# Optimization experiments

Measured on AMD Instinct MI355X. Metric: run time of the kernel, lower is better.

The kernel has to match this reference:

```python
import jax, jax.numpy as jnp
import numpy as np

B, S, D, H, L, I, V, T = 8, 512, 768, 12, 6, 3072, 30522, 2
DH = D // H  # 64


def ln2d(x, g, b, eps=1e-5):
    # LayerNorm over the last two dims ([S, D]), affine params shaped [S, D]
    mu = jnp.mean(x, axis=(-2, -1), keepdims=True)
    var = jnp.var(x, axis=(-2, -1), keepdims=True)
    return (x - mu) * jax.lax.rsqrt(var + eps) * g + b


def setup_inputs() -> dict:
    key = jax.random.key(0)
    ks = jax.random.split(key, 16)
    s = 0.02
    inp = {
        "input_ids": jax.random.randint(ks[0], (B, S), 0, V, dtype=jnp.int32),
        "segment_ids": jax.random.randint(ks[1], (B, S), 0, T, dtype=jnp.int32),
        "input_mask": jnp.ones((B, S), dtype=jnp.float32),
        "word_emb": jax.random.normal(ks[2], (V, D), jnp.float32) * s,
        "seg_emb": jax.random.normal(ks[3], (T, D), jnp.float32) * s,
        "pos_emb": jax.random.normal(ks[4], (S, D), jnp.float32) * s,
        "ln0_g": jnp.ones((S, D), jnp.float32),
        "ln0_b": jnp.zeros((S, D), jnp.float32),
        "Wq": jax.random.normal(ks[5], (L, D, D), jnp.float32) * s,
        "Wk": jax.random.normal(ks[6], (L, D, D), jnp.float32) * s,
        "Wv": jax.random.normal(ks[7], (L, D, D), jnp.float32) * s,
        "W1": jax.random.normal(ks[8], (L, D, D), jnp.float32) * s,
        "b1": jnp.zeros((L, D), jnp.float32),
        "Wi": jax.random.normal(ks[9], (L, D, I), jnp.float32) * s,
        "bi": jnp.zeros((L, I), jnp.float32),
        "W2": jax.random.normal(ks[10], (L, I, D), jnp.float32) * s,
        "b2": jnp.zeros((L, D), jnp.float32),
        "lng": jnp.ones((L, S, D), jnp.float32),
        "lnb": jnp.zeros((L, S, D), jnp.float32),
        "Wp": jax.random.normal(ks[11], (D, 2), jnp.float32) * s,
        "bp": jnp.zeros((2,), jnp.float32),
    }
    return inp


def _forward(input_ids, segment_ids, input_mask, word_emb, seg_emb, pos_emb,
             ln0_g, ln0_b, Wq, Wk, Wv, W1, b1, Wi, bi, W2, b2, lng, lnb, Wp, bp):
    # embedding (word + segment + position), then 2-D LayerNorm
    x = word_emb[input_ids] + seg_emb[segment_ids] + pos_emb  # [B,S,D]
    x = ln2d(x, ln0_g, ln0_b)
    # multiplicative attention mask, broadcast over heads and KEY axis
    qmask = input_mask[:, None, :, None]  # [B,1,S,1]
    scale = 1.0 / jnp.sqrt(jnp.asarray(DH, x.dtype))
    for l in range(L):
        prev = x
        q = (x @ Wq[l]).reshape(B, S, H, DH).transpose(0, 2, 1, 3)
        k = (x @ Wk[l]).reshape(B, S, H, DH).transpose(0, 2, 1, 3)
        v = (x @ Wv[l]).reshape(B, S, H, DH).transpose(0, 2, 1, 3)
        scores = jnp.einsum('bhqd,bhkd->bhqk', q, k) * scale
        scores = scores * qmask  # multiplicative mask (as in source)
        probs = jax.nn.softmax(scores, axis=-1)
        attn = jnp.einsum('bhqk,bhkd->bhqd', probs, v)
        attn = attn.transpose(0, 2, 1, 3).reshape(B, S, D)
        h = jax.nn.relu(attn @ W1[l] + b1[l])
        h = jax.nn.relu(h @ Wi[l] + bi[l])
        h = jax.nn.relu(h @ W2[l] + b2[l])
        x = ln2d(h + prev, lng[l], lnb[l])
    logits = x @ Wp + bp  # [B,S,2]
    logits = logits + (1.0 - input_mask)[:, :, None] * (-1e4)
    return logits[:, :, 0], logits[:, :, 1]


def reference(input_ids, segment_ids, input_mask, word_emb, seg_emb, pos_emb,
              ln0_g, ln0_b, Wq, Wk, Wv, W1, b1, Wi, bi, W2, b2, lng, lnb, Wp, bp):
    return _forward(input_ids, segment_ids, input_mask, word_emb, seg_emb, pos_emb,
                    ln0_g, ln0_b, Wq, Wk, Wv, W1, b1, Wi, bi, W2, b2, lng, lnb, Wp, bp)
```

## Files before the change

### kernel.cpp

```cpp
#include <hip/hip_runtime.h>
#include <cstdint>
#include <cstddef>

typedef __bf16 bf16x8 __attribute__((ext_vector_type(8)));
typedef float f32x4 __attribute__((ext_vector_type(4)));
typedef unsigned short u16;

#define NB 8
#define NS 512
#define ND 768
#define NH 12
#define NL 6
#define NI 3072
#define NROWS (NB*NS)
#define SD (NS*ND)
#define MN ((size_t)NROWS*ND)

__device__ __forceinline__ u16 f2bf(float f) {
  union { float f; unsigned u; } v; v.f = f;
  unsigned r = v.u + 0x7fffu + ((v.u >> 16) & 1u);
  return (u16)(r >> 16);
}
__device__ __forceinline__ float b2f(u16 u) {
  union { unsigned u; float f; } v; v.u = ((unsigned)u) << 16; return v.f;
}

#define GLL(gsrc, ldst) \
  __builtin_amdgcn_global_load_lds((__attribute__((address_space(1))) void*)(gsrc), \
                                   (__attribute__((address_space(3))) void*)(ldst), 16, 0, 0)

#define CHS 4168

__global__ __launch_bounds__(256) void wconv_k(
    const float* __restrict__ Wq, const float* __restrict__ Wk, const float* __restrict__ Wv,
    const float* __restrict__ W1, const float* __restrict__ Wi, const float* __restrict__ W2,
    u16* __restrict__ wqkv_t, u16* __restrict__ w1_t, u16* __restrict__ wi_t, u16* __restrict__ w2_t)
{
  int bid = blockIdx.x;
  int l = bid / 864, r = bid % 864;
  const float* src; u16* dst; int Csrc, dstLD, tr, tc;
  if (r < 216) {
    int which = r / 72, t2 = r % 72;
    src = (which == 0 ? Wq : (which == 1 ? Wk : Wv)) + (size_t)l * ND * ND;
    dst = wqkv_t + (size_t)l * 2304 * ND + (size_t)which * ND * ND;
    Csrc = ND; dstLD = ND; tr = t2 / 12; tc = t2 % 12;
  } else if (r < 288) {
    int t2 = r - 216;
    src = W1 + (size_t)l * ND * ND; dst = w1_t + (size_t)l * ND * ND;
    Csrc = ND; dstLD = ND; tr = t2 / 12; tc = t2 % 12;
  } else if (r < 576) {
    int t2 = r - 288;
    src = Wi + (size_t)l * ND * NI; dst = wi_t + (size_t)l * ND * NI;
    Csrc = NI; dstLD = ND; tr = t2 / 48; tc = t2 % 48;
  } else {
    int t2 = r - 576;
    src = W2 + (size_t)l * ND * NI; dst = w2_t + (size_t)l * ND * NI;
    Csrc = ND; dstLD = NI; tr = t2 / 12; tc = t2 % 12;
  }
  __shared__ u16 lds[2 * CHS];
  int t0 = threadIdx.x;
  {
    int rrow = t0 >> 3, c0 = (t0 & 7) * 8;
    float4 va[4], vb[4];
    #pragma unroll
    for (int q = 0; q < 4; q++) {
      const float* sp = src + (size_t)(tr * 128 + q * 32 + rrow) * Csrc + tc * 64 + c0;
      va[q] = *reinterpret_cast<const float4*>(sp);
      vb[q] = *reinterpret_cast<const float4*>(sp + 4);
    }
    #pragma unroll
    for (int q = 0; q < 4; q++) {
      int row = q * 32 + rrow;
      u16* lp = &lds[(row >> 6) * CHS + (row & 63) * 65 + c0];
      lp[0] = f2bf(va[q].x); lp[1] = f2bf(va[q].y); lp[2] = f2bf(va[q].z); lp[3] = f2bf(va[q].w);
      lp[4] = f2bf(vb[q].x); lp[5] = f2bf(vb[q].y); lp[6] = f2bf(vb[q].z); lp[7] = f2bf(vb[q].w);
    }
  }
  __syncthreads();
  {
    int qq = t0 & 15;
    int rb = t0 >> 4;
    int ch = qq >> 3;
    int r6b = (qq & 7) * 8;
    #pragma unroll
    for (int p = 0; p < 4; p++) {
      int dstrow = p * 16 + rb;
      const u16* lq = &lds[ch * CHS + dstrow];
      unsigned res[4];
      #pragma unroll
      for (int e = 0; e < 4; e++) {
        unsigned lo = lq[(r6b + 2 * e) * 65];
        unsigned hi = lq[(r6b + 2 * e + 1) * 65];
        res[e] = lo | (hi << 16);
      }
      u16* dp = dst + (size_t)(tc * 64 + dstrow) * dstLD + tr * 128 + qq * 8;
      *reinterpret_cast<uint4*>(dp) = make_uint4(res[0], res[1], res[2], res[3]);
    }
  }
}

__global__ __launch_bounds__(256) void embed_ln_k(const int* __restrict__ ids,
    const int* __restrict__ segs, const float* __restrict__ wemb,
    const float* __restrict__ semb, const float* __restrict__ pemb,
    float* __restrict__ out, float* __restrict__ part)
{
  int b = blockIdx.x >> 6, c = blockIdx.x & 63;
  int base_row = b * NS + c * 8;
  int t = threadIdx.x;
  float s = 0.f, sq = 0.f;
  #pragma unroll
  for (int j = 0; j < 6; j++) {
    int fi = t + j * 256;
    int riw = fi / 192, col4 = fi - riw * 192;
    int row = base_row + riw;
    int id = ids[row], sg = segs[row];
    int srow = row & (NS - 1);
    float4 a = reinterpret_cast<const float4*>(wemb + (size_t)id * ND)[col4];
    float4 bb = reinterpret_cast<const float4*>(semb + (size_t)sg * ND)[col4];
    float4 cc = reinterpret_cast<const float4*>(pemb + (size_t)srow * ND)[col4];
    float y0 = a.x + bb.x + cc.x, y1 = a.y + bb.y + cc.y;
    float y2 = a.z + bb.z + cc.z, y3 = a.w + bb.w + cc.w;
    float4 o; o.x = y0; o.y = y1; o.z = y2; o.w = y3;
    reinterpret_cast<float4*>(out)[(size_t)row * 192 + col4] = o;
    s += y0 + y1 + y2 + y3;
    sq += y0 * y0 + y1 * y1 + y2 * y2 + y3 * y3;
  }
  #pragma unroll
  for (int d = 1; d < 64; d <<= 1) { s += __shfl_xor(s, d); sq += __shfl_xor(sq, d); }
  __shared__ float red[8];
  int w = t >> 6, lane = t & 63;
  if (lane == 0) { red[w] = s; red[4 + w] = sq; }
  __syncthreads();
  if (t == 0) {
    part[blockIdx.x * 2 + 0] = red[0] + red[1] + red[2] + red[3];
    part[blockIdx.x * 2 + 1] = red[4] + red[5] + red[6] + red[7];
  }
}

__global__ __launch_bounds__(256) void ln_apply_k(const float* __restrict__ x,
    const float* __restrict__ g, const float* __restrict__ bta, const float* __restrict__ part,
    u16* __restrict__ xb)
{
  int idx = blockIdx.x * 256 + threadIdx.x;
  int e = idx * 4;
  int b = e / SD;
  int sd = e - b * SD;
  int lane = threadIdx.x & 63;
  float s = part[b * 128 + lane * 2 + 0];
  float q = part[b * 128 + lane * 2 + 1];
  #pragma unroll
  for (int d = 1; d < 64; d <<= 1) { s += __shfl_xor(s, d); q += __shfl_xor(q, d); }
  float inv = 1.f / (float)SD;
  float mu = s * inv;
  float rstd = rsqrtf(q * inv - mu * mu + 1e-5f);
  float4 v = reinterpret_cast<const float4*>(x)[idx];
  float4 gg = reinterpret_cast<const float4*>(g)[sd >> 2];
  float4 bb = reinterpret_cast<const float4*>(bta)[sd >> 2];
  float y0 = (v.x - mu) * rstd * gg.x + bb.x;
  float y1 = (v.y - mu) * rstd * gg.y + bb.y;
  float y2 = (v.z - mu) * rstd * gg.z + bb.z;
  float y3 = (v.w - mu) * rstd * gg.w + bb.w;
  reinterpret_cast<ushort4*>(xb)[idx] = make_ushort4(f2bf(y0), f2bf(y1), f2bf(y2), f2bf(y3));
}

__global__ __launch_bounds__(256) void finw1_k(const float* __restrict__ P,
    const float* __restrict__ bias, u16* __restrict__ out)
{
  size_t idx = (size_t)blockIdx.x * 256 + threadIdx.x;
  float4 p0 = reinterpret_cast<const float4*>(P)[idx];
  float4 p1 = reinterpret_cast<const float4*>(P)[idx + (MN >> 2)];
  float4 p2 = reinterpret_cast<const float4*>(P)[idx + 2 * (MN >> 2)];
  float4 p3 = reinterpret_cast<const float4*>(P)[idx + 3 * (MN >> 2)];
  int col4 = (int)((idx * 4) % ND) >> 2;
  float4 bv = reinterpret_cast<const float4*>(bias)[col4];
  float y0 = fmaxf(p0.x + p1.x + p2.x + p3.x + bv.x, 0.f);
  float y1 = fmaxf(p0.y + p1.y + p2.y + p3.y + bv.y, 0.f);
  float y2 = fmaxf(p0.z + p1.z + p2.z + p3.z + bv.z, 0.f);
  float y3 = fmaxf(p0.w + p1.w + p2.w + p3.w + bv.w, 0.f);
  reinterpret_cast<ushort4*>(out)[idx] = make_ushort4(f2bf(y0), f2bf(y1), f2bf(y2), f2bf(y3));
}

__global__ __launch_bounds__(256) void finw2_k(const float* __restrict__ P,
    const float* __restrict__ bias, const u16* __restrict__ resid,
    float* __restrict__ ln_in, float* __restrict__ part)
{
  int b = blockIdx.x >> 6, c = blockIdx.x & 63;
  size_t f4base = ((size_t)b * SD + (size_t)c * 6144) >> 2;
  int t = threadIdx.x;
  float s = 0.f, sq = 0.f;
  #pragma unroll
  for (int j = 0; j < 6; j++) {
    size_t fi = f4base + t + j * 256;
    float4 p0 = reinterpret_cast<const float4*>(P)[fi];
    float4 p1 = reinterpret_cast<const float4*>(P)[fi + (MN >> 2)];
    float4 p2 = reinterpret_cast<const float4*>(P)[fi + 2 * (MN >> 2)];
    float4 p3 = reinterpret_cast<const float4*>(P)[fi + 3 * (MN >> 2)];
    ushort4 rv = reinterpret_cast<const ushort4*>(resid)[fi];
    int col4 = (((t + j * 256) * 4) % ND) >> 2;
    float4 bv = reinterpret_cast<const float4*>(bias)[col4];
    float y0 = fmaxf(p0.x + p1.x + p2.x + p3.x + bv.x, 0.f) + b2f(rv.x);
    float y1 = fmaxf(p0.y + p1.y + p2.y + p3.y + bv.y, 0.f) + b2f(rv.y);
    float y2 = fmaxf(p0.z + p1.z + p2.z + p3.z + bv.z, 0.f) + b2f(rv.z);
    float y3 = fmaxf(p0.w + p1.w + p2.w + p3.w + bv.w, 0.f) + b2f(rv.w);
    float4 o; o.x = y0; o.y = y1; o.z = y2; o.w = y3;
    reinterpret_cast<float4*>(ln_in)[fi] = o;
    s += y0 + y1 + y2 + y3;
    sq += y0 * y0 + y1 * y1 + y2 * y2 + y3 * y3;
  }
  #pragma unroll
  for (int d = 1; d < 64; d <<= 1) { s += __shfl_xor(s, d); sq += __shfl_xor(sq, d); }
  __shared__ float red[8];
  int w = t >> 6, lane = t & 63;
  if (lane == 0) { red[w] = s; red[4 + w] = sq; }
  __syncthreads();
  if (t == 0) {
    part[blockIdx.x * 2 + 0] = red[0] + red[1] + red[2] + red[3];
    part[blockIdx.x * 2 + 1] = red[4] + red[5] + red[6] + red[7];
  }
}

#define BM 128
#define BN 128
#define BK 32

template<int EPI>
__global__ __launch_bounds__(256) void gemm_bt(
    const u16* __restrict__ A, const u16* __restrict__ Bt, void* __restrict__ Cv,
    const float* __restrict__ bias, int M, int N, int K)
{
  __shared__ __align__(16) u16 As[2][BM * BK];
  __shared__ __align__(16) u16 Bs[2][BN * BK];
  const int t = threadIdx.x;
  const int lane = t & 63, w = t >> 6;
  const int wr = w >> 1, wc = w & 1;
  const int l15 = lane & 15, lh = lane >> 4;
  const int m0 = blockIdx.y * BM, n0 = blockIdx.x * BN;
  const int Ksub = K / gridDim.z;
  const int Koff = blockIdx.z * Ksub;

  f32x4 acc[4][4];
  const f32x4 z4 = {0.f, 0.f, 0.f, 0.f};
  #pragma unroll
  for (int i = 0; i < 4; i++)
    #pragma unroll
    for (int j = 0; j < 4; j++) acc[i][j] = z4;

  const int ca = t, cb = t + 256;
  const u16* a0p = A + (size_t)(m0 + (ca >> 2)) * K + (ca & 3) * 8 + Koff;
  const u16* a1p = A + (size_t)(m0 + (cb >> 2)) * K + (cb & 3) * 8 + Koff;
  const u16* b0p = Bt + (size_t)(n0 + (ca >> 2)) * K + (ca & 3) * 8 + Koff;
  const u16* b1p = Bt + (size_t)(n0 + (cb >> 2)) * K + (cb & 3) * 8 + Koff;

  auto stage = [&](int buf, int k0) {
    GLL(a0p + k0, &As[buf][ca * 8]);
    GLL(a1p + k0, &As[buf][cb * 8]);
    GLL(b0p + k0, &Bs[buf][ca * 8]);
    GLL(b1p + k0, &Bs[buf][cb * 8]);
  };

  const int nt = Ksub / BK;
  stage(0, 0);
  __syncthreads();
  for (int it = 0; it < nt; ++it) {
    const int cur = it & 1;
    if (it + 1 < nt) stage(cur ^ 1, (it + 1) * BK);
    bf16x8 af[4], bfr[4];
    #pragma unroll
    for (int i = 0; i < 4; i++)
      af[i] = *reinterpret_cast<const bf16x8*>(&As[cur][(wr * 64 + i * 16 + l15) * BK + lh * 8]);
    #pragma unroll
    for (int j = 0; j < 4; j++)
      bfr[j] = *reinterpret_cast<const bf16x8*>(&Bs[cur][(wc * 64 + j * 16 + l15) * BK + lh * 8]);
    #pragma unroll
    for (int i = 0; i < 4; i++)
      #pragma unroll
      for (int j = 0; j < 4; j++)
        acc[i][j] = __builtin_amdgcn_mfma_f32_16x16x32_bf16(af[i], bfr[j], acc[i][j], 0, 0, 0);
    __syncthreads();
  }

  float* Pout = (float*)Cv + (size_t)blockIdx.z * M * N;
  #pragma unroll
  for (int i = 0; i < 4; i++) {
    int row_b = m0 + wr * 64 + i * 16 + lh * 4;
    #pragma unroll
    for (int j = 0; j < 4; j++) {
      int col = n0 + wc * 64 + j * 16 + l15;
      float bv = (EPI == 1) ? bias[col] : 0.f;
      #pragma unroll
      for (int r = 0; r < 4; r++) {
        size_t off = (size_t)(row_b + r) * N + col;
        float v = acc[i][j][r];
        if (EPI == 1) ((u16*)Cv)[off] = f2bf(fmaxf(v + bv, 0.f));
        else if (EPI == 3) Pout[off] = v;
        else ((u16*)Cv)[off] = f2bf(v);
      }
    }
  }
}

__global__ __launch_bounds__(256) void attn_k(
    const u16* __restrict__ qkv, const float* __restrict__ mask, u16* __restrict__ out)
{
  const int qt = blockIdx.x;
  const int h = blockIdx.y;
  const int b = blockIdx.z;
  __shared__ __align__(16) u16 Qs[64 * 64];
  __shared__ __align__(16) u16 Ks[64 * 72];
  __shared__ __align__(16) u16 Vt[64 * 72];
  __shared__ __align__(16) u16 Pw[4][16 * 72];
  const int t = threadIdx.x, lane = t & 63, w = t >> 6;
  const int l15 = lane & 15, lh = lane >> 4;

  #pragma unroll
  for (int p = 0; p < 2; p++) {
    int c = t + p * 256;
    const u16* src = qkv + (size_t)(b * NS + qt * 64 + (c >> 3)) * 2304 + h * 64 + (c & 7) * 8;
    GLL(src, Qs + c * 8);
  }
  __syncthreads();

  bf16x8 aq[2];
  #pragma unroll
  for (int kk = 0; kk < 2; kk++)
    aq[kk] = *reinterpret_cast<const bf16x8*>(&Qs[(w * 16 + l15) * 64 + kk * 32 + lh * 8]);

  float qm[4];
  #pragma unroll
  for (int r = 0; r < 4; r++)
    qm[r] = mask[b * NS + qt * 64 + w * 16 + lh * 4 + r] * 0.125f;

  float mrun[4], lrun[4];
  f32x4 o[4];
  const f32x4 z4 = {0.f, 0.f, 0.f, 0.f};
  #pragma unroll
  for (int r = 0; r < 4; r++) { mrun[r] = -3e38f; lrun[r] = 0.f; }
  #pragma unroll
  for (int jn = 0; jn < 4; jn++) o[jn] = z4;

  for (int kc = 0; kc < 8; kc++) {
    __syncthreads();
    #pragma unroll
    for (int p = 0; p < 2; p++) {
      int k = (t >> 3) + p * 32;
      int dh0 = (t & 7) * 8;
      const u16* ks = qkv + (size_t)(b * NS + kc * 64 + k) * 2304 + ND + h * 64 + dh0;
      uint4 kv4 = *reinterpret_cast<const uint4*>(ks);
      *reinterpret_cast<uint4*>(&Ks[k * 72 + dh0]) = kv4;
    }
    #pragma unroll
    for (int p = 0; p < 2; p++) {
      int k = (t >> 3) + p * 32;
      int dh0 = (t & 7) * 8;
      const u16* vs = qkv + (size_t)(b * NS + kc * 64 + k) * 2304 + 2 * ND + h * 64 + dh0;
      uint4 vv = *reinterpret_cast<const uint4*>(vs);
      Vt[(dh0 + 0) * 72 + k] = (u16)(vv.x & 0xffff);
      Vt[(dh0 + 1) * 72 + k] = (u16)(vv.x >> 16);
      Vt[(dh0 + 2) * 72 + k] = (u16)(vv.y & 0xffff);
      Vt[(dh0 + 3) * 72 + k] = (u16)(vv.y >> 16);
      Vt[(dh0 + 4) * 72 + k] = (u16)(vv.z & 0xffff);
      Vt[(dh0 + 5) * 72 + k] = (u16)(vv.z >> 16);
      Vt[(dh0 + 6) * 72 + k] = (u16)(vv.w & 0xffff);
      Vt[(dh0 + 7) * 72 + k] = (u16)(vv.w >> 16);
    }
    __syncthreads();

    f32x4 s[4];
    #pragma unroll
    for (int j = 0; j < 4; j++) s[j] = z4;
    #pragma unroll
    for (int kk = 0; kk < 2; kk++) {
      bf16x8 bk[4];
      #pragma unroll
      for (int j = 0; j < 4; j++)
        bk[j] = *reinterpret_cast<const bf16x8*>(&Ks[(j * 16 + l15) * 72 + kk * 32 + lh * 8]);
      #pragma unroll
      for (int j = 0; j < 4; j++)
        s[j] = __builtin_amdgcn_mfma_f32_16x16x32_bf16(aq[kk], bk[j], s[j], 0, 0, 0);
    }

    #pragma unroll
    for (int r = 0; r < 4; r++) {
      float q4 = qm[r];
      float v0 = s[0][r] * q4, v1 = s[1][r] * q4, v2 = s[2][r] * q4, v3 = s[3][r] * q4;
      float pm = fmaxf(fmaxf(v0, v1), fmaxf(v2, v3));
      pm = fmaxf(pm, __shfl_xor(pm, 1));
      pm = fmaxf(pm, __shfl_xor(pm, 2));
      pm = fmaxf(pm, __shfl_xor(pm, 4));
      pm = fmaxf(pm, __shfl_xor(pm, 8));
      float mnew = fmaxf(mrun[r], pm);
      float corr = __expf(mrun[r] - mnew);
      mrun[r] = mnew;
      float p0 = __expf(v0 - mnew), p1 = __expf(v1 - mnew);
      float p2 = __expf(v2 - mnew), p3 = __expf(v3 - mnew);
      s[0][r] = p0; s[1][r] = p1; s[2][r] = p2; s[3][r] = p3;
      float rs = p0 + p1 + p2 + p3;
      rs += __shfl_xor(rs, 1);
      rs += __shfl_xor(rs, 2);
      rs += __shfl_xor(rs, 4);
      rs += __shfl_xor(rs, 8);
      lrun[r] = lrun[r] * corr + rs;
      #pragma unroll
      for (int jn = 0; jn < 4; jn++) o[jn][r] *= corr;
    }
    #pragma unroll
    for (int j = 0; j < 4; j++)
      #pragma unroll
      for (int r = 0; r < 4; r++)
        Pw[w][(lh * 4 + r) * 72 + j * 16 + l15] = f2bf(s[j][r]);

    #pragma unroll
    for (int kk2 = 0; kk2 < 2; kk2++) {
      bf16x8 pa, vb[4];
      pa = *reinterpret_cast<const bf16x8*>(&Pw[w][l15 * 72 + kk2 * 32 + lh * 8]);
      #pragma unroll
      for (int jn = 0; jn < 4; jn++)
        vb[jn] = *reinterpret_cast<const bf16x8*>(&Vt[(jn * 16 + l15) * 72 + kk2 * 32 + lh * 8]);
      #pragma unroll
      for (int jn = 0; jn < 4; jn++)
        o[jn] = __builtin_amdgcn_mfma_f32_16x16x32_bf16(pa, vb[jn], o[jn], 0, 0, 0);
    }
  }

  #pragma unroll
  for (int r = 0; r < 4; r++) {
    int q = qt * 64 + w * 16 + lh * 4 + r;
    float invl = 1.f / lrun[r];
    #pragma unroll
    for (int jn = 0; jn < 4; jn++) {
      int col = h * 64 + jn * 16 + l15;
      out[(size_t)(b * NS + q) * ND + col] = f2bf(o[jn][r] * invl);
    }
  }
}

__global__ __launch_bounds__(256) void logits_k(const u16* __restrict__ x,
    const float* __restrict__ Wp, const float* __restrict__ bp, const float* __restrict__ mask,
    float* __restrict__ out)
{
  int t = threadIdx.x, lane = t & 63, w = t >> 6;
  int row = blockIdx.x * 4 + w;
  const u16* xr = x + (size_t)row * ND;
  float a0 = 0.f, a1 = 0.f;
  for (int i = lane; i < ND; i += 64) {
    float v = b2f(xr[i]);
    a0 += v * Wp[i * 2 + 0];
    a1 += v * Wp[i * 2 + 1];
  }
  #pragma unroll
  for (int d = 1; d < 64; d <<= 1) { a0 += __shfl_xor(a0, d); a1 += __shfl_xor(a1, d); }
  if (lane == 0) {
    float pen = (1.f - mask[row]) * -10000.f;
    out[row] = a0 + bp[0] + pen;
    out[NROWS + row] = a1 + bp[1] + pen;
  }
}

extern "C" void kernel_launch(void* const* d_in, const int* in_sizes, int n_in,
                              void* d_out, int out_size, void* d_ws, size_t ws_size,
                              hipStream_t stream)
{
  const int* ids = (const int*)d_in[0];
  const int* segs = (const int*)d_in[1];
  const float* mask = (const float*)d_in[2];
  const float* wemb = (const float*)d_in[3];
  const float* semb = (const float*)d_in[4];
  const float* pemb = (const float*)d_in[5];
  const float* ln0g = (const float*)d_in[6];
  const float* ln0b = (const float*)d_in[7];
  const float* Wq = (const float*)d_in[8];
  const float* Wk = (const float*)d_in[9];
  const float* Wv = (const float*)d_in[10];
  const float* W1 = (const float*)d_in[11];
  const float* b1 = (const float*)d_in[12];
  const float* Wi = (const float*)d_in[13];
  const float* bi = (const float*)d_in[14];
  const float* W2 = (const float*)d_in[15];
  const float* b2 = (const float*)d_in[16];
  const float* lng = (const float*)d_in[17];
  const float* lnb = (const float*)d_in[18];
  const float* Wp = (const float*)d_in[19];
  const float* bp = (const float*)d_in[20];

  char* ws = (char*)d_ws;
  size_t o = 0;
  auto alloc = [&](size_t n) { size_t r = o; o += (n + 255) & ~(size_t)255; return r; };
  u16* wqkv_t = (u16*)(ws + alloc((size_t)NL * 2304 * ND * 2));
  u16* w1_t   = (u16*)(ws + alloc((size_t)NL * ND * ND * 2));
  u16* wi_t   = (u16*)(ws + alloc((size_t)NL * ND * NI * 2));
  u16* w2_t   = (u16*)(ws + alloc((size_t)NL * ND * NI * 2));
  u16* x_bf16  = (u16*)(ws + alloc((size_t)NROWS * ND * 2));
  u16* qkv     = (u16*)(ws + alloc((size_t)NROWS * 2304 * 2));
  u16* attn    = (u16*)(ws + alloc((size_t)NROWS * ND * 2));
  u16* h1      = (u16*)(ws + alloc((size_t)NROWS * ND * 2));
  u16* hi      = (u16*)(ws + alloc((size_t)NROWS * NI * 2));
  float* ln_in = (float*)(ws + alloc((size_t)NROWS * ND * 4));
  float* pbuf  = (float*)(ws + alloc(4 * MN * 4));
  float* part  = (float*)(ws + alloc(512 * 2 * 4));

  wconv_k<<<NL * 864, 256, 0, stream>>>(Wq, Wk, Wv, W1, Wi, W2, wqkv_t, w1_t, wi_t, w2_t);
  embed_ln_k<<<512, 256, 0, stream>>>(ids, segs, wemb, semb, pemb, ln_in, part);
  ln_apply_k<<<3072, 256, 0, stream>>>(ln_in, ln0g, ln0b, part, x_bf16);

  for (int l = 0; l < NL; l++) {
    gemm_bt<0><<<dim3(18, 32), 256, 0, stream>>>(x_bf16, wqkv_t + (size_t)l * 2304 * ND, qkv,
                                                 nullptr, NROWS, 2304, ND);
    attn_k<<<dim3(8, NH, NB), 256, 0, stream>>>(qkv, mask, attn);
    gemm_bt<3><<<dim3(6, 32, 4), 256, 0, stream>>>(attn, w1_t + (size_t)l * ND * ND, pbuf,
                                                   nullptr, NROWS, ND, ND);
    finw1_k<<<3072, 256, 0, stream>>>(pbuf, b1 + (size_t)l * ND, h1);
    gemm_bt<1><<<dim3(24, 32), 256, 0, stream>>>(h1, wi_t + (size_t)l * ND * NI, hi,
                                                 bi + (size_t)l * NI, NROWS, NI, ND);
    gemm_bt<3><<<dim3(6, 32, 4), 256, 0, stream>>>(hi, w2_t + (size_t)l * ND * NI, pbuf,
                                                   nullptr, NROWS, ND, NI);
    finw2_k<<<512, 256, 0, stream>>>(pbuf, b2 + (size_t)l * ND, x_bf16, ln_in, part);
    ln_apply_k<<<3072, 256, 0, stream>>>(ln_in, lng + (size_t)l * SD, lnb + (size_t)l * SD, part, x_bf16);
  }

  logits_k<<<1024, 256, 0, stream>>>(x_bf16, Wp, bp, mask, (float*)d_out);
}
```

Before: 1.115 ms.

## Store split-K partials in bf16 and remap workgroups across XCDs

The split-K GEMM partial buffers now hold bf16 instead of fp32, which halves the write and read traffic between the split-K GEMMs and their finishing kernels. Workgroup IDs in the GEMM and attention kernels are also remapped so that consecutive logical tiles land on the same XCD, aiming to improve L2 locality on the multi-die MI355X. Rounding each partial sum to bf16 before reduction lowers accuracy.

```diff
diff --git a/kernel.cpp b/kernel.cpp
--- a/kernel.cpp
+++ b/kernel.cpp
@@ -163,24 +163,24 @@
   reinterpret_cast<ushort4*>(xb)[idx] = make_ushort4(f2bf(y0), f2bf(y1), f2bf(y2), f2bf(y3));
 }
 
-__global__ __launch_bounds__(256) void finw1_k(const float* __restrict__ P,
+__global__ __launch_bounds__(256) void finw1_k(const u16* __restrict__ P,
     const float* __restrict__ bias, u16* __restrict__ out)
 {
   size_t idx = (size_t)blockIdx.x * 256 + threadIdx.x;
-  float4 p0 = reinterpret_cast<const float4*>(P)[idx];
-  float4 p1 = reinterpret_cast<const float4*>(P)[idx + (MN >> 2)];
-  float4 p2 = reinterpret_cast<const float4*>(P)[idx + 2 * (MN >> 2)];
-  float4 p3 = reinterpret_cast<const float4*>(P)[idx + 3 * (MN >> 2)];
+  ushort4 p0 = reinterpret_cast<const ushort4*>(P)[idx];
+  ushort4 p1 = reinterpret_cast<const ushort4*>(P)[idx + (MN >> 2)];
+  ushort4 p2 = reinterpret_cast<const ushort4*>(P)[idx + 2 * (MN >> 2)];
+  ushort4 p3 = reinterpret_cast<const ushort4*>(P)[idx + 3 * (MN >> 2)];
   int col4 = (int)((idx * 4) % ND) >> 2;
   float4 bv = reinterpret_cast<const float4*>(bias)[col4];
-  float y0 = fmaxf(p0.x + p1.x + p2.x + p3.x + bv.x, 0.f);
-  float y1 = fmaxf(p0.y + p1.y + p2.y + p3.y + bv.y, 0.f);
-  float y2 = fmaxf(p0.z + p1.z + p2.z + p3.z + bv.z, 0.f);
-  float y3 = fmaxf(p0.w + p1.w + p2.w + p3.w + bv.w, 0.f);
+  float y0 = fmaxf(b2f(p0.x) + b2f(p1.x) + b2f(p2.x) + b2f(p3.x) + bv.x, 0.f);
+  float y1 = fmaxf(b2f(p0.y) + b2f(p1.y) + b2f(p2.y) + b2f(p3.y) + bv.y, 0.f);
+  float y2 = fmaxf(b2f(p0.z) + b2f(p1.z) + b2f(p2.z) + b2f(p3.z) + bv.z, 0.f);
+  float y3 = fmaxf(b2f(p0.w) + b2f(p1.w) + b2f(p2.w) + b2f(p3.w) + bv.w, 0.f);
   reinterpret_cast<ushort4*>(out)[idx] = make_ushort4(f2bf(y0), f2bf(y1), f2bf(y2), f2bf(y3));
 }
 
-__global__ __launch_bounds__(256) void finw2_k(const float* __restrict__ P,
+__global__ __launch_bounds__(256) void finw2_k(const u16* __restrict__ P,
     const float* __restrict__ bias, const u16* __restrict__ resid,
     float* __restrict__ ln_in, float* __restrict__ part)
 {
@@ -191,17 +191,17 @@
   #pragma unroll
   for (int j = 0; j < 6; j++) {
     size_t fi = f4base + t + j * 256;
-    float4 p0 = reinterpret_cast<const float4*>(P)[fi];
-    float4 p1 = reinterpret_cast<const float4*>(P)[fi + (MN >> 2)];
-    float4 p2 = reinterpret_cast<const float4*>(P)[fi + 2 * (MN >> 2)];
-    float4 p3 = reinterpret_cast<const float4*>(P)[fi + 3 * (MN >> 2)];
+    ushort4 p0 = reinterpret_cast<const ushort4*>(P)[fi];
+    ushort4 p1 = reinterpret_cast<const ushort4*>(P)[fi + (MN >> 2)];
+    ushort4 p2 = reinterpret_cast<const ushort4*>(P)[fi + 2 * (MN >> 2)];
+    ushort4 p3 = reinterpret_cast<const ushort4*>(P)[fi + 3 * (MN >> 2)];
     ushort4 rv = reinterpret_cast<const ushort4*>(resid)[fi];
     int col4 = (((t + j * 256) * 4) % ND) >> 2;
     float4 bv = reinterpret_cast<const float4*>(bias)[col4];
-    float y0 = fmaxf(p0.x + p1.x + p2.x + p3.x + bv.x, 0.f) + b2f(rv.x);
-    float y1 = fmaxf(p0.y + p1.y + p2.y + p3.y + bv.y, 0.f) + b2f(rv.y);
-    float y2 = fmaxf(p0.z + p1.z + p2.z + p3.z + bv.z, 0.f) + b2f(rv.z);
-    float y3 = fmaxf(p0.w + p1.w + p2.w + p3.w + bv.w, 0.f) + b2f(rv.w);
+    float y0 = fmaxf(b2f(p0.x) + b2f(p1.x) + b2f(p2.x) + b2f(p3.x) + bv.x, 0.f) + b2f(rv.x);
+    float y1 = fmaxf(b2f(p0.y) + b2f(p1.y) + b2f(p2.y) + b2f(p3.y) + bv.y, 0.f) + b2f(rv.y);
+    float y2 = fmaxf(b2f(p0.z) + b2f(p1.z) + b2f(p2.z) + b2f(p3.z) + bv.z, 0.f) + b2f(rv.z);
+    float y3 = fmaxf(b2f(p0.w) + b2f(p1.w) + b2f(p2.w) + b2f(p3.w) + bv.w, 0.f) + b2f(rv.w);
     float4 o; o.x = y0; o.y = y1; o.z = y2; o.w = y3;
     reinterpret_cast<float4*>(ln_in)[fi] = o;
     s += y0 + y1 + y2 + y3;
@@ -230,13 +230,19 @@
 {
   __shared__ __align__(16) u16 As[2][BM * BK];
   __shared__ __align__(16) u16 Bs[2][BN * BK];
+  const int gx = gridDim.x, gy = gridDim.y;
+  int wg = (blockIdx.z * gy + blockIdx.y) * gx + blockIdx.x;
+  int nwg = gx * gy * gridDim.z;
+  int L = (wg & 7) * (nwg >> 3) + (wg >> 3);
+  const int bx = L % gx, by = (L / gx) % gy, bz = L / (gx * gy);
+
   const int t = threadIdx.x;
   const int lane = t & 63, w = t >> 6;
   const int wr = w >> 1, wc = w & 1;
   const int l15 = lane & 15, lh = lane >> 4;
-  const int m0 = blockIdx.y * BM, n0 = blockIdx.x * BN;
+  const int m0 = by * BM, n0 = bx * BN;
   const int Ksub = K / gridDim.z;
-  const int Koff = blockIdx.z * Ksub;
+  const int Koff = bz * Ksub;
 
   f32x4 acc[4][4];
   const f32x4 z4 = {0.f, 0.f, 0.f, 0.f};
@@ -279,7 +285,7 @@
     __syncthreads();
   }
 
-  float* Pout = (float*)Cv + (size_t)blockIdx.z * M * N;
+  u16* PoutB = (u16*)Cv + (size_t)bz * M * N;
   #pragma unroll
   for (int i = 0; i < 4; i++) {
     int row_b = m0 + wr * 64 + i * 16 + lh * 4;
@@ -292,7 +298,7 @@
         size_t off = (size_t)(row_b + r) * N + col;
         float v = acc[i][j][r];
         if (EPI == 1) ((u16*)Cv)[off] = f2bf(fmaxf(v + bv, 0.f));
-        else if (EPI == 3) Pout[off] = v;
+        else if (EPI == 3) PoutB[off] = f2bf(v);
         else ((u16*)Cv)[off] = f2bf(v);
       }
     }
@@ -302,9 +308,11 @@
 __global__ __launch_bounds__(256) void attn_k(
     const u16* __restrict__ qkv, const float* __restrict__ mask, u16* __restrict__ out)
 {
-  const int qt = blockIdx.x;
-  const int h = blockIdx.y;
-  const int b = blockIdx.z;
+  int wg = (blockIdx.z * 12 + blockIdx.y) * 8 + blockIdx.x;
+  int L = (wg & 7) * 96 + (wg >> 3);
+  const int qt = L & 7;
+  const int h = (L >> 3) % 12;
+  const int b = L / 96;
   __shared__ __align__(16) u16 Qs[64 * 64];
   __shared__ __align__(16) u16 Ks[64 * 72];
   __shared__ __align__(16) u16 Vt[64 * 72];
@@ -495,7 +503,7 @@
   u16* h1      = (u16*)(ws + alloc((size_t)NROWS * ND * 2));
   u16* hi      = (u16*)(ws + alloc((size_t)NROWS * NI * 2));
   float* ln_in = (float*)(ws + alloc((size_t)NROWS * ND * 4));
-  float* pbuf  = (float*)(ws + alloc(4 * MN * 4));
+  u16* pbuf    = (u16*)(ws + alloc(4 * MN * 2));
   float* part  = (float*)(ws + alloc(512 * 2 * 4));
 
   wconv_k<<<NL * 864, 256, 0, stream>>>(Wq, Wk, Wv, W1, Wi, W2, wqkv_t, w1_t, wi_t, w2_t);
```

Result: faster. 976.3 us (-12.4%).
